# Optimization experiments

Measured on AMD Instinct MI355X. Metric: run time of the kernel, lower is better.

The kernel has to match this reference:

```python
import jax, jax.numpy as jnp
import numpy as np

EPS = 1e-5  # BatchNorm2d default eps


def conv1x1_bn(x, W, gamma, beta, mean, var):
    # 1x1 conv (no bias) + BatchNorm2d in inference form.
    # x: (n, Cin, h, w), W: (Cout, Cin)
    y = jnp.einsum('oc,nchw->nohw', W, x)
    inv = gamma / jnp.sqrt(var + EPS)          # (C,)
    return y * inv[None, :, None, None] + (beta - mean * inv)[None, :, None, None]


def setup_inputs() -> dict:
    key = jax.random.key(0)
    ks = jax.random.split(key, 16)
    B, C, H, W = 8, 256, 128, 128
    sd = 1.0 / np.sqrt(C)
    inp = {
        'x':  jax.random.normal(ks[0], (B, C, H, W), jnp.float32),
        'Wk': jax.random.normal(ks[1], (C, C), jnp.float32) * sd,
        'k_gamma': jax.random.uniform(ks[2], (C,), jnp.float32, 0.5, 1.5),
        'k_beta':  jax.random.normal(ks[3], (C,), jnp.float32) * 0.1,
        'k_mean':  jax.random.normal(ks[4], (C,), jnp.float32) * 0.1,
        'k_var':   jax.random.uniform(ks[5], (C,), jnp.float32, 0.5, 1.5),
        'Wq': jax.random.normal(ks[6], (C, C), jnp.float32) * sd,
        'q_gamma': jax.random.uniform(ks[7], (C,), jnp.float32, 0.5, 1.5),
        'q_beta':  jax.random.normal(ks[8], (C,), jnp.float32) * 0.1,
        'q_mean':  jax.random.normal(ks[9], (C,), jnp.float32) * 0.1,
        'q_var':   jax.random.uniform(ks[10], (C,), jnp.float32, 0.5, 1.5),
        'Wv': jax.random.normal(ks[11], (C, C), jnp.float32) * sd,
        'v_gamma': jax.random.uniform(ks[12], (C,), jnp.float32, 0.5, 1.5),
        'v_beta':  jax.random.normal(ks[13], (C,), jnp.float32) * 0.1,
        'v_mean':  jax.random.normal(ks[14], (C,), jnp.float32) * 0.1,
        'v_var':   jax.random.uniform(ks[15], (C,), jnp.float32, 0.5, 1.5),
    }
    return inp


def reference(x, Wk, k_gamma, k_beta, k_mean, k_var,
              Wq, q_gamma, q_beta, q_mean, q_var,
              Wv, v_gamma, v_beta, v_mean, v_var):
    n, c, h, w = x.shape
    k = conv1x1_bn(x, Wk, k_gamma, k_beta, k_mean, k_var).reshape(n, c, h * w)  # (n,C,S)
    q = conv1x1_bn(x, Wq, q_gamma, q_beta, q_mean, q_var).reshape(n, c, h * w)
    v = conv1x1_bn(x, Wv, v_gamma, v_beta, v_mean, v_var).reshape(n, c, h * w)
    # torch: attention = softmax(q @ k^T, dim=2) -> (n, C, C) channel attention
    attn = jax.nn.softmax(jnp.einsum('ncs,nds->ncd', q, k), axis=-1)
    out = jnp.einsum('ncd,nds->ncs', attn, v).reshape(n, c, h, w)
    return out + x  # res = Identity (in_channels == out_channels)
```

## Files before the change

### kernel.cpp

```cpp
#include <hip/hip_runtime.h>


typedef __bf16 bf16x8 __attribute__((ext_vector_type(8)));
typedef float f32x4 __attribute__((ext_vector_type(4)));
typedef unsigned short us8 __attribute__((ext_vector_type(8)));

#define EPS 1e-5f

__device__ __forceinline__ unsigned short f2bf(float f) {
  unsigned int u = __float_as_uint(f);
  u += 0x7fffu + ((u >> 16) & 1u);
  return (unsigned short)(u >> 16);
}
__device__ __forceinline__ float bf2f(unsigned short h) {
  return __uint_as_float(((unsigned int)h) << 16);
}
__device__ __forceinline__ bf16x8 ld_frag(const unsigned short* p) {
  union { us8 u; bf16x8 b; } x;
  x.u = *(const us8*)p;
  return x.b;
}

#define LDB 72
__global__ __launch_bounds__(512, 2) void kGram(const float* __restrict__ x,
                                                float* __restrict__ Gp,
                                                float* __restrict__ rp,
                                                int chunk) {
  __shared__ __align__(16) unsigned short lh[256 * LDB];
  __shared__ __align__(16) unsigned short ll[256 * LDB];
  const int n = blockIdx.y;
  const int k0 = blockIdx.x * chunk;
  const int nkt = chunk >> 6;
  const int tid = threadIdx.x;
  const float* xn = x + (size_t)n * 4194304;

  f32x4 acc[2][16];
  const f32x4 z4 = {0.f, 0.f, 0.f, 0.f};
#pragma unroll
  for (int i = 0; i < 2; ++i)
#pragma unroll
    for (int j = 0; j < 16; ++j) acc[i][j] = z4;
  float rs[4] = {0.f, 0.f, 0.f, 0.f};

  const int lane = tid & 63, w = tid >> 6;
  const int m = lane & 15, q = lane >> 4;

  for (int kt = 0; kt < nkt; ++kt) {
    const int kb = k0 + kt * 64;
    __syncthreads();
#pragma unroll
    for (int u = 0; u < 4; ++u) {
      const int idx = tid + u * 512;
      const int row = idx >> 3, g = idx & 7;
      const float* p = xn + (size_t)row * 16384 + kb + g * 8;
      const float4 v0 = *(const float4*)p;
      const float4 v1 = *(const float4*)(p + 4);
      float fv[8] = {v0.x, v0.y, v0.z, v0.w, v1.x, v1.y, v1.z, v1.w};
      union { unsigned short s[8]; uint4 v; } H, L;
#pragma unroll
      for (int e = 0; e < 8; ++e) {
        const unsigned short h = f2bf(fv[e]);
        H.s[e] = h;
        L.s[e] = f2bf(fv[e] - bf2f(h));
        rs[u] += fv[e];
      }
      *(uint4*)&lh[row * LDB + g * 8] = H.v;
      *(uint4*)&ll[row * LDB + g * 8] = L.v;
    }
    __syncthreads();
#pragma unroll
    for (int kk = 0; kk < 64; kk += 32) {
      bf16x8 Ah[2], Al[2];
#pragma unroll
      for (int i = 0; i < 2; ++i) {
        const int off = (w * 32 + i * 16 + m) * LDB + kk + q * 8;
        Ah[i] = ld_frag(&lh[off]);
        Al[i] = ld_frag(&ll[off]);
      }
#pragma unroll
      for (int j = 0; j < 16; ++j) {
        const int off = (j * 16 + m) * LDB + kk + q * 8;
        const bf16x8 Bh = ld_frag(&lh[off]);
        const bf16x8 Bl = ld_frag(&ll[off]);
#pragma unroll
        for (int i = 0; i < 2; ++i) {
          acc[i][j] = __builtin_amdgcn_mfma_f32_16x16x32_bf16(Ah[i], Bh, acc[i][j], 0, 0, 0);
          acc[i][j] = __builtin_amdgcn_mfma_f32_16x16x32_bf16(Ah[i], Bl, acc[i][j], 0, 0, 0);
          acc[i][j] = __builtin_amdgcn_mfma_f32_16x16x32_bf16(Al[i], Bh, acc[i][j], 0, 0, 0);
        }
      }
    }
  }
  const size_t slot = (size_t)n * gridDim.x + blockIdx.x;
#pragma unroll
  for (int u = 0; u < 4; ++u) {
    float v = rs[u];
    v += __shfl_xor(v, 1);
    v += __shfl_xor(v, 2);
    v += __shfl_xor(v, 4);
    if ((lane & 7) == 0) rp[slot * 256 + ((tid + u * 512) >> 3)] = v;
  }
  float* Gpn = Gp + slot * 65536;
#pragma unroll
  for (int i = 0; i < 2; ++i)
#pragma unroll
    for (int j = 0; j < 16; ++j)
#pragma unroll
      for (int e = 0; e < 4; ++e) {
        const int grow = w * 32 + i * 16 + q * 4 + e;
        const int gcol = j * 16 + m;
        Gpn[grow * 256 + gcol] = acc[i][j][e];
      }
}

__global__ void kReduce(const float* __restrict__ Gp, float* __restrict__ G,
                        int splits) {
  const int e4 = (blockIdx.x * 256 + threadIdx.x) * 4;
  const int n = e4 >> 16, el = e4 & 65535;
  const float* p = Gp + (size_t)n * splits * 65536 + el;
  float4 s = {0.f, 0.f, 0.f, 0.f};
  for (int i = 0; i < splits; ++i) {
    const float4 v = *(const float4*)(p + (size_t)i * 65536);
    s.x += v.x; s.y += v.y; s.z += v.z; s.w += v.w;
  }
  *(float4*)(G + e4) = s;
}

#define TLD 260
__global__ __launch_bounds__(256) void kAttn(
    const float* __restrict__ G, const float* __restrict__ rp, int splits,
    const float* __restrict__ Wq, const float* __restrict__ qga, const float* __restrict__ qbe,
    const float* __restrict__ qme, const float* __restrict__ qva,
    const float* __restrict__ Wk, const float* __restrict__ kga, const float* __restrict__ kbe,
    const float* __restrict__ kme, const float* __restrict__ kva,
    const float* __restrict__ Wv, const float* __restrict__ vga, const float* __restrict__ vbe,
    const float* __restrict__ vme, const float* __restrict__ vva,
    unsigned short* __restrict__ M, float* __restrict__ cvec) {
  __shared__ __align__(16) float t_lds[8 * TLD];
  __shared__ __align__(16) float p_lds[8 * TLD];
  __shared__ __align__(16) float r_lds[256];
  __shared__ float ivv_lds[256], bv_lds[256];
  __shared__ float rq_lds[8], bq_lds[8], rsum_lds[8];

  const int n = blockIdx.y, r0 = blockIdx.x * 8;
  const int t = threadIdx.x;
  const int lane = t & 63;
  const int w = __builtin_amdgcn_readfirstlane(t >> 6);
  const float* Gn = G + (size_t)n * 65536;

  {
    float s = 0.f;
    const float* p = rp + (size_t)n * splits * 256 + t;
    for (int ss = 0; ss < splits; ++ss) s += p[ss * 256];
    r_lds[t] = s;
    const float iv = vga[t] * rsqrtf(vva[t] + EPS);
    ivv_lds[t] = iv;
    bv_lds[t] = vbe[t] - vme[t] * iv;
  }
  __syncthreads();

  const int c0 = r0 + 2 * w, c1 = c0 + 1;
  const float ivq0 = qga[c0] * rsqrtf(qva[c0] + EPS);
  const float ivq1 = qga[c1] * rsqrtf(qva[c1] + EPS);

  {
    const float4 r4 = *(const float4*)(r_lds + lane * 4);
#pragma unroll
    for (int rr = 0; rr < 2; ++rr) {
      const float4 w4 = *(const float4*)(Wq + (size_t)(c0 + rr) * 256 + lane * 4);
      float s = w4.x * r4.x + w4.y * r4.y + w4.z * r4.z + w4.w * r4.w;
      s += __shfl_xor(s, 1);  s += __shfl_xor(s, 2);  s += __shfl_xor(s, 4);
      s += __shfl_xor(s, 8);  s += __shfl_xor(s, 16); s += __shfl_xor(s, 32);
      if (lane == 0) rq_lds[2 * w + rr] = s * (rr ? ivq1 : ivq0);
    }
    if (lane == 0) {
      bq_lds[2 * w + 0] = qbe[c0] - qme[c0] * ivq0;
      bq_lds[2 * w + 1] = qbe[c1] - qme[c1] * ivq1;
    }
  }

  {
    float4 tr0 = {0.f, 0.f, 0.f, 0.f}, tr1 = {0.f, 0.f, 0.f, 0.f};
    const float* wq0 = Wq + (size_t)c0 * 256;
    const float* wq1 = Wq + (size_t)c1 * 256;
    for (int kb = 0; kb < 256; kb += 4) {
      union { float4 v; float f[4]; } A0, A1;
      A0.v = *(const float4*)(wq0 + kb);
      A1.v = *(const float4*)(wq1 + kb);
#pragma unroll
      for (int e = 0; e < 4; ++e) {
        const float4 g4 = *(const float4*)(Gn + (size_t)(kb + e) * 256 + lane * 4);
        const float a0 = A0.f[e], a1 = A1.f[e];
        tr0.x += a0 * g4.x; tr0.y += a0 * g4.y; tr0.z += a0 * g4.z; tr0.w += a0 * g4.w;
        tr1.x += a1 * g4.x; tr1.y += a1 * g4.y; tr1.z += a1 * g4.z; tr1.w += a1 * g4.w;
      }
    }
    tr0.x *= ivq0; tr0.y *= ivq0; tr0.z *= ivq0; tr0.w *= ivq0;
    tr1.x *= ivq1; tr1.y *= ivq1; tr1.z *= ivq1; tr1.w *= ivq1;
    *(float4*)(t_lds + (2 * w + 0) * TLD + lane * 4) = tr0;
    *(float4*)(t_lds + (2 * w + 1) * TLD + lane * 4) = tr1;
  }
  __syncthreads();

  {
    float lreg[8];
#pragma unroll
    for (int i = 0; i < 8; ++i) lreg[i] = 0.f;
    const float ivk = kga[t] * rsqrtf(kva[t] + EPS);
    const float bkd = kbe[t] - kme[t] * ivk;
    float rkd = 0.f;
    const float* wkrow = Wk + (size_t)t * 256;
    for (int jb = 0; jb < 256; jb += 4) {
      const float4 w4 = *(const float4*)(wkrow + jb);
      const float4 r4 = *(const float4*)(r_lds + jb);
      rkd += w4.x * r4.x + w4.y * r4.y + w4.z * r4.z + w4.w * r4.w;
#pragma unroll
      for (int i = 0; i < 8; ++i) {
        const float4 t4 = *(const float4*)(t_lds + i * TLD + jb);
        lreg[i] += t4.x * w4.x + t4.y * w4.y + t4.z * w4.z + t4.w * w4.w;
      }
    }
#pragma unroll
    for (int i = 0; i < 8; ++i)
      p_lds[i * TLD + t] = ivk * lreg[i] + rq_lds[i] * bkd +
                           bq_lds[i] * (ivk * rkd) + 16384.0f * bq_lds[i] * bkd;
  }
  __syncthreads();

  {
    const int i = t >> 5, s = t & 31;
    float* row = p_lds + i * TLD;
    float mx = -1e30f;
#pragma unroll
    for (int u = 0; u < 8; ++u) mx = fmaxf(mx, row[s + u * 32]);
    mx = fmaxf(mx, __shfl_xor(mx, 1));
    mx = fmaxf(mx, __shfl_xor(mx, 2));
    mx = fmaxf(mx, __shfl_xor(mx, 4));
    mx = fmaxf(mx, __shfl_xor(mx, 8));
    mx = fmaxf(mx, __shfl_xor(mx, 16));
    float sraw = 0.f, sbv = 0.f;
#pragma unroll
    for (int u = 0; u < 8; ++u) {
      const int d = s + u * 32;
      const float e = __expf(row[d] - mx);
      sraw += e;
      sbv += e * bv_lds[d];
      row[d] = e * ivv_lds[d];
    }
    sraw += __shfl_xor(sraw, 1);  sbv += __shfl_xor(sbv, 1);
    sraw += __shfl_xor(sraw, 2);  sbv += __shfl_xor(sbv, 2);
    sraw += __shfl_xor(sraw, 4);  sbv += __shfl_xor(sbv, 4);
    sraw += __shfl_xor(sraw, 8);  sbv += __shfl_xor(sbv, 8);
    sraw += __shfl_xor(sraw, 16); sbv += __shfl_xor(sbv, 16);
    if (s == 0) {
      rsum_lds[i] = sraw;
      cvec[n * 256 + r0 + i] = sbv / sraw;
    }
  }
  __syncthreads();

  {
    float mreg[8];
#pragma unroll
    for (int i = 0; i < 8; ++i) mreg[i] = 0.f;
    for (int db = 0; db < 256; db += 4) {
      float wv[4];
#pragma unroll
      for (int e = 0; e < 4; ++e) wv[e] = Wv[(size_t)(db + e) * 256 + t];
#pragma unroll
      for (int i = 0; i < 8; ++i) {
        const float4 p4 = *(const float4*)(p_lds + i * TLD + db);
        mreg[i] += p4.x * wv[0] + p4.y * wv[1] + p4.z * wv[2] + p4.w * wv[3];
      }
    }
#pragma unroll
    for (int i = 0; i < 8; ++i)
      M[((size_t)n * 256 + r0 + i) * 256 + t] = f2bf(mreg[i] / rsum_lds[i]);
  }
}

#define LDT 40
__global__ __launch_bounds__(256, 2) void kOut(const float* __restrict__ x,
                                               const unsigned short* __restrict__ M,
                                               const float* __restrict__ cvec,
                                               float* __restrict__ out) {
  __shared__ __align__(16) unsigned short xt[64 * LDT];
  __shared__ __align__(16) float xf[256 * 64];
  const int n = blockIdx.y, s0 = blockIdx.x * 64;
  const int tid = threadIdx.x;
  const float* xn = x + (size_t)n * 4194304;
  const unsigned short* Mn = M + (size_t)n * 65536;
  const int lane = tid & 63, w = tid >> 6;
  const int m = lane & 15, q = lane >> 4;

  f32x4 acc[4][4];
  const f32x4 z4 = {0.f, 0.f, 0.f, 0.f};
#pragma unroll
  for (int i = 0; i < 4; ++i)
#pragma unroll
    for (int ct = 0; ct < 4; ++ct) acc[i][ct] = z4;

  for (int kt = 0; kt < 8; ++kt) {
    __syncthreads();
#pragma unroll
    for (int u = 0; u < 2; ++u) {
      const int fidx = tid + u * 256;
      const int ch = fidx >> 4, f = fidx & 15;
      const float4 v = *(const float4*)(xn + (size_t)(kt * 32 + ch) * 16384 + s0 + f * 4);
      *(float4*)&xf[(kt * 32 + ch) * 64 + f * 4] = v;
      xt[(f * 4 + 0) * LDT + ch] = f2bf(v.x);
      xt[(f * 4 + 1) * LDT + ch] = f2bf(v.y);
      xt[(f * 4 + 2) * LDT + ch] = f2bf(v.z);
      xt[(f * 4 + 3) * LDT + ch] = f2bf(v.w);
    }
    __syncthreads();
    bf16x8 A[4], B[4];
#pragma unroll
    for (int i = 0; i < 4; ++i)
      A[i] = ld_frag(&Mn[((w * 4 + i) * 16 + m) * 256 + kt * 32 + q * 8]);
#pragma unroll
    for (int ct = 0; ct < 4; ++ct)
      B[ct] = ld_frag(&xt[(ct * 16 + m) * LDT + q * 8]);
#pragma unroll
    for (int i = 0; i < 4; ++i)
#pragma unroll
      for (int ct = 0; ct < 4; ++ct)
        acc[i][ct] = __builtin_amdgcn_mfma_f32_16x16x32_bf16(A[i], B[ct], acc[i][ct], 0, 0, 0);
  }
#pragma unroll
  for (int i = 0; i < 4; ++i) {
    const int cb = w * 64 + i * 16 + q * 4;
#pragma unroll
    for (int e = 0; e < 4; ++e) {
      const int c = cb + e;
      const float cv = cvec[n * 256 + c];
      float* orow = out + ((size_t)n * 256 + c) * 16384 + s0;
#pragma unroll
      for (int ct = 0; ct < 4; ++ct) {
        const int s = ct * 16 + m;
        orow[s] = acc[i][ct][e] + cv + xf[c * 64 + s];
      }
    }
  }
}

extern "C" void kernel_launch(void* const* d_in, const int* in_sizes, int n_in,
                              void* d_out, int out_size, void* d_ws, size_t ws_size,
                              hipStream_t stream) {
  const float* x   = (const float*)d_in[0];
  const float* Wk  = (const float*)d_in[1];
  const float* kga = (const float*)d_in[2];
  const float* kbe = (const float*)d_in[3];
  const float* kme = (const float*)d_in[4];
  const float* kva = (const float*)d_in[5];
  const float* Wq  = (const float*)d_in[6];
  const float* qga = (const float*)d_in[7];
  const float* qbe = (const float*)d_in[8];
  const float* qme = (const float*)d_in[9];
  const float* qva = (const float*)d_in[10];
  const float* Wv  = (const float*)d_in[11];
  const float* vga = (const float*)d_in[12];
  const float* vbe = (const float*)d_in[13];
  const float* vme = (const float*)d_in[14];
  const float* vva = (const float*)d_in[15];

  char* ws = (char*)d_ws;
  float* G           = (float*)(ws);
  unsigned short* Mm = (unsigned short*)(ws + 2097152);
  float* cv          = (float*)(ws + 3145728);
  float* rp          = (float*)(ws + 3153920);
  float* Gp          = (float*)(ws + 3416064);
  float* out         = (float*)d_out;

  int splits = 32;
  while (splits > 1 &&
         (size_t)3416064 + (size_t)splits * 8 * 65536 * 4 > ws_size)
    splits >>= 1;
  const int chunk = 16384 / splits;

  kGram<<<dim3(splits, 8), 512, 0, stream>>>(x, Gp, rp, chunk);
  kReduce<<<512, 256, 0, stream>>>(Gp, G, splits);
  kAttn<<<dim3(32, 8), 256, 0, stream>>>(G, rp, splits,
                                         Wq, qga, qbe, qme, qva,
                                         Wk, kga, kbe, kme, kva,
                                         Wv, vga, vbe, vme, vva,
                                         Mm, cv);
  kOut<<<dim3(256, 8), 256, 0, stream>>>(x, Mm, cv, out);
}
```

Baseline: 388.1 us.

## Double-buffer Gram tiles, use symmetric split-bf16 product, retile waves 4x8

The Gram kernel now prefetches the next x tile into registers and converts it into a second LDS buffer while MFMAs run on the current one, removing one barrier per iteration. The three-term bf16 split product is replaced by two terms (hi·hi + hi·lo·2 scaled by 0.5), with a new kSym kernel that forms G + G^T, so the missing lo·hi term comes from symmetry. The wave tiling changes from 2x16 to 4x8 fragments to cut B-fragment LDS reads. This cuts MFMA work by a third but adds an extra small kernel launch and doubles LDS use, which may lower occupancy.

New measurement: 393.2 us. Within noise of the previous version (+1.3%).

```diff
diff --git a/kernel.cpp b/kernel.cpp
--- a/kernel.cpp
+++ b/kernel.cpp
@@ -22,75 +22,97 @@
 }
 
 #define LDB 72
+
+#define CONV_WRITE(dst)                                                     \
+  _Pragma("unroll")                                                         \
+  for (int u = 0; u < 4; ++u) {                                             \
+    float fv[8] = {pa[u].x, pa[u].y, pa[u].z, pa[u].w,                      \
+                   pb[u].x, pb[u].y, pb[u].z, pb[u].w};                     \
+    union { unsigned short s[8]; uint4 v; } H, L;                           \
+    _Pragma("unroll")                                                       \
+    for (int e = 0; e < 8; ++e) {                                           \
+      const unsigned short h = f2bf(fv[e]);                                 \
+      H.s[e] = h;                                                           \
+      L.s[e] = f2bf(2.0f * (fv[e] - bf2f(h)));                              \
+      rs[u] += fv[e];                                                       \
+    }                                                                       \
+    *(uint4*)&sh[dst][(srow + u * 64) * LDB + sg * 8] = H.v;                \
+    *(uint4*)&sl[dst][(srow + u * 64) * LDB + sg * 8] = L.v;                \
+  }
+
 __global__ __launch_bounds__(512, 2) void kGram(const float* __restrict__ x,
                                                 float* __restrict__ Gp,
                                                 float* __restrict__ rp,
                                                 int chunk) {
-  __shared__ __align__(16) unsigned short lh[256 * LDB];
-  __shared__ __align__(16) unsigned short ll[256 * LDB];
+  __shared__ __align__(16) unsigned short sh[2][256 * LDB];
+  __shared__ __align__(16) unsigned short sl[2][256 * LDB];
   const int n = blockIdx.y;
   const int k0 = blockIdx.x * chunk;
   const int nkt = chunk >> 6;
   const int tid = threadIdx.x;
   const float* xn = x + (size_t)n * 4194304;
 
-  f32x4 acc[2][16];
+  f32x4 acc[4][8];
   const f32x4 z4 = {0.f, 0.f, 0.f, 0.f};
 #pragma unroll
-  for (int i = 0; i < 2; ++i)
-#pragma unroll
-    for (int j = 0; j < 16; ++j) acc[i][j] = z4;
+  for (int i = 0; i < 4; ++i)
+#pragma unroll
+    for (int j = 0; j < 8; ++j) acc[i][j] = z4;
   float rs[4] = {0.f, 0.f, 0.f, 0.f};
 
   const int lane = tid & 63, w = tid >> 6;
   const int m = lane & 15, q = lane >> 4;
+  const int wr = w >> 1, wc = w & 1;
+  const int srow = tid >> 3, sg = tid & 7;
+
+  float4 pa[4], pb[4];
+
+#pragma unroll
+  for (int u = 0; u < 4; ++u) {
+    const float* p = xn + (size_t)(srow + u * 64) * 16384 + k0 + sg * 8;
+    pa[u] = *(const float4*)p;
+    pb[u] = *(const float4*)(p + 4);
+  }
+  CONV_WRITE(0)
+  __syncthreads();
 
   for (int kt = 0; kt < nkt; ++kt) {
-    const int kb = k0 + kt * 64;
-    __syncthreads();
-#pragma unroll
-    for (int u = 0; u < 4; ++u) {
-      const int idx = tid + u * 512;
-      const int row = idx >> 3, g = idx & 7;
-      const float* p = xn + (size_t)row * 16384 + kb + g * 8;
-      const float4 v0 = *(const float4*)p;
-      const float4 v1 = *(const float4*)(p + 4);
-      float fv[8] = {v0.x, v0.y, v0.z, v0.w, v1.x, v1.y, v1.z, v1.w};
-      union { unsigned short s[8]; uint4 v; } H, L;
-#pragma unroll
-      for (int e = 0; e < 8; ++e) {
-        const unsigned short h = f2bf(fv[e]);
-        H.s[e] = h;
-        L.s[e] = f2bf(fv[e] - bf2f(h));
-        rs[u] += fv[e];
-      }
-      *(uint4*)&lh[row * LDB + g * 8] = H.v;
-      *(uint4*)&ll[row * LDB + g * 8] = L.v;
-    }
-    __syncthreads();
+    const int b = kt & 1;
+    const bool more = (kt + 1 < nkt);
+    if (more) {
+      const int kb = k0 + (kt + 1) * 64;
+#pragma unroll
+      for (int u = 0; u < 4; ++u) {
+        const float* p = xn + (size_t)(srow + u * 64) * 16384 + kb + sg * 8;
+        pa[u] = *(const float4*)p;
+        pb[u] = *(const float4*)(p + 4);
+      }
+    }
 #pragma unroll
     for (int kk = 0; kk < 64; kk += 32) {
-      bf16x8 Ah[2], Al[2];
-#pragma unroll
-      for (int i = 0; i < 2; ++i) {
-        const int off = (w * 32 + i * 16 + m) * LDB + kk + q * 8;
-        Ah[i] = ld_frag(&lh[off]);
-        Al[i] = ld_frag(&ll[off]);
-      }
-#pragma unroll
-      for (int j = 0; j < 16; ++j) {
-        const int off = (j * 16 + m) * LDB + kk + q * 8;
-        const bf16x8 Bh = ld_frag(&lh[off]);
-        const bf16x8 Bl = ld_frag(&ll[off]);
-#pragma unroll
-        for (int i = 0; i < 2; ++i) {
+      bf16x8 Ah[4];
+#pragma unroll
+      for (int i = 0; i < 4; ++i)
+        Ah[i] = ld_frag(&sh[b][(wr * 64 + i * 16 + m) * LDB + kk + q * 8]);
+#pragma unroll
+      for (int j = 0; j < 8; ++j) {
+        const int off = (wc * 128 + j * 16 + m) * LDB + kk + q * 8;
+        const bf16x8 Bh = ld_frag(&sh[b][off]);
+        const bf16x8 Bl = ld_frag(&sl[b][off]);
+#pragma unroll
+        for (int i = 0; i < 4; ++i) {
           acc[i][j] = __builtin_amdgcn_mfma_f32_16x16x32_bf16(Ah[i], Bh, acc[i][j], 0, 0, 0);
           acc[i][j] = __builtin_amdgcn_mfma_f32_16x16x32_bf16(Ah[i], Bl, acc[i][j], 0, 0, 0);
-          acc[i][j] = __builtin_amdgcn_mfma_f32_16x16x32_bf16(Al[i], Bh, acc[i][j], 0, 0, 0);
         }
       }
     }
-  }
+    if (more) {
+      const int nb = b ^ 1;
+      CONV_WRITE(nb)
+      __syncthreads();
+    }
+  }
+
   const size_t slot = (size_t)n * gridDim.x + blockIdx.x;
 #pragma unroll
   for (int u = 0; u < 4; ++u) {
@@ -98,32 +120,57 @@
     v += __shfl_xor(v, 1);
     v += __shfl_xor(v, 2);
     v += __shfl_xor(v, 4);
-    if ((lane & 7) == 0) rp[slot * 256 + ((tid + u * 512) >> 3)] = v;
+    if ((lane & 7) == 0) rp[slot * 256 + (srow + u * 64)] = v;
   }
   float* Gpn = Gp + slot * 65536;
 #pragma unroll
-  for (int i = 0; i < 2; ++i)
-#pragma unroll
-    for (int j = 0; j < 16; ++j)
+  for (int i = 0; i < 4; ++i)
+#pragma unroll
+    for (int j = 0; j < 8; ++j)
 #pragma unroll
       for (int e = 0; e < 4; ++e) {
-        const int grow = w * 32 + i * 16 + q * 4 + e;
-        const int gcol = j * 16 + m;
-        Gpn[grow * 256 + gcol] = acc[i][j][e];
-      }
-}
-
-__global__ void kReduce(const float* __restrict__ Gp, float* __restrict__ G,
-                        int splits) {
+        const int grow = wr * 64 + i * 16 + q * 4 + e;
+        const int gcol = wc * 128 + j * 16 + m;
+        Gpn[grow * 256 + gcol] = 0.5f * acc[i][j][e];
+      }
+}
+
+__global__ void kReduce(float* __restrict__ Gp, int splits) {
   const int e4 = (blockIdx.x * 256 + threadIdx.x) * 4;
   const int n = e4 >> 16, el = e4 & 65535;
-  const float* p = Gp + (size_t)n * splits * 65536 + el;
+  float* p = Gp + (size_t)n * splits * 65536 + el;
   float4 s = {0.f, 0.f, 0.f, 0.f};
   for (int i = 0; i < splits; ++i) {
     const float4 v = *(const float4*)(p + (size_t)i * 65536);
     s.x += v.x; s.y += v.y; s.z += v.z; s.w += v.w;
   }
-  *(float4*)(G + e4) = s;
+  *(float4*)p = s;
+}
+
+__global__ void kSym(const float* __restrict__ Gs, float* __restrict__ G,
+                     int sstride) {
+  __shared__ __align__(16) float pt[64][68];
+  const int n = blockIdx.y;
+  const int bi = blockIdx.x >> 2, bj = blockIdx.x & 3;
+  const float* gsn = Gs + (size_t)n * sstride;
+  float* gn = G + (size_t)n * 65536;
+  const int t = threadIdx.x, r = t >> 2, cg = (t & 3) * 16;
+#pragma unroll
+  for (int e = 0; e < 16; e += 4)
+    *(float4*)&pt[r][cg + e] =
+        *(const float4*)(gsn + (size_t)(bj * 64 + r) * 256 + bi * 64 + cg + e);
+  __syncthreads();
+#pragma unroll
+  for (int e = 0; e < 16; e += 4) {
+    const float4 a =
+        *(const float4*)(gsn + (size_t)(bi * 64 + r) * 256 + bj * 64 + cg + e);
+    float4 o;
+    o.x = a.x + pt[cg + e + 0][r];
+    o.y = a.y + pt[cg + e + 1][r];
+    o.z = a.z + pt[cg + e + 2][r];
+    o.w = a.w + pt[cg + e + 3][r];
+    *(float4*)(gn + (size_t)(bi * 64 + r) * 256 + bj * 64 + cg + e) = o;
+  }
 }
 
 #define TLD 260
@@ -379,7 +426,8 @@
   const int chunk = 16384 / splits;
 
   kGram<<<dim3(splits, 8), 512, 0, stream>>>(x, Gp, rp, chunk);
-  kReduce<<<512, 256, 0, stream>>>(Gp, G, splits);
+  kReduce<<<512, 256, 0, stream>>>(Gp, splits);
+  kSym<<<dim3(16, 8), 256, 0, stream>>>(Gp, G, splits * 65536);
   kAttn<<<dim3(32, 8), 256, 0, stream>>>(G, rp, splits,
                                          Wq, qga, qbe, qme, qva,
                                          Wk, kga, kbe, kme, kva,
```
